# Performance work log

Measured on AMD Instinct MI355X. Metric: run time of the kernel, lower is better.

Reference implementation:

```python
import jax, jax.numpy as jnp
import numpy as np

B, T, C, H = 8, 1024, 768, 12
D = C // H  # head dim = 64


def setup_inputs() -> dict:
    key = jax.random.key(0)
    ks = jax.random.split(key, 5)
    x = jax.random.normal(ks[0], (B, T, C), dtype=jnp.float32)
    W_attn = jax.random.normal(ks[1], (C, 3 * C), dtype=jnp.float32) * 0.02
    b_attn = jnp.zeros((3 * C,), dtype=jnp.float32)
    W_proj = jax.random.normal(ks[2], (C, C), dtype=jnp.float32) * 0.02
    b_proj = jnp.zeros((C,), dtype=jnp.float32)
    return {"x": x, "W_attn": W_attn, "b_attn": b_attn, "W_proj": W_proj, "b_proj": b_proj}


def reference(x, W_attn, b_attn, W_proj, b_proj):
    Bx, Tx, Cx = x.shape
    qkv = x @ W_attn + b_attn                      # [B,T,3C]
    q, k, v = jnp.split(qkv, 3, axis=-1)           # each [B,T,C]
    # [B,T,C] -> [B,H,T,D]
    q = q.reshape(Bx, Tx, H, D).transpose(0, 2, 1, 3)
    k = k.reshape(Bx, Tx, H, D).transpose(0, 2, 1, 3)
    v = v.reshape(Bx, Tx, H, D).transpose(0, 2, 1, 3)
    scale = 1.0 / jnp.sqrt(jnp.asarray(D, dtype=x.dtype))
    att = jnp.einsum('bhqd,bhkd->bhqk', q, k) * scale   # [B,H,T,T]
    causal = jnp.tril(jnp.ones((Tx, Tx), dtype=bool))    # [T,T]
    att = jnp.where(causal[None, None, :, :], att, jnp.asarray(-jnp.inf, dtype=att.dtype))
    att = jax.nn.softmax(att, axis=-1)
    y = jnp.einsum('bhqk,bhkd->bhqd', att, v)            # [B,H,T,D]
    y = y.transpose(0, 2, 1, 3).reshape(Bx, Tx, Cx)      # [B,T,C]
    return y @ W_proj + b_proj
```

## Files before the change

kernel.cpp:

```cpp
#include <hip/hip_runtime.h>
#include <stdint.h>

typedef short short8 __attribute__((ext_vector_type(8)));
typedef float f32x4 __attribute__((ext_vector_type(4)));

__device__ __forceinline__ unsigned short f2bf(float f) {
    union { float f; uint32_t u; } v; v.f = f;
    uint32_t u = v.u;
    u += 0x7FFFu + ((u >> 16) & 1u);
    return (unsigned short)(u >> 16);
}

__device__ __forceinline__ void gload_lds16(const void* g, void* l) {
    __builtin_amdgcn_global_load_lds(
        (const __attribute__((address_space(1))) void*)g,
        (__attribute__((address_space(3))) void*)l, 16, 0, 0);
}

__global__ void k_f32_to_bf16(const float* __restrict__ in, unsigned short* __restrict__ out, int n4) {
    int i = blockIdx.x * blockDim.x + threadIdx.x;
    if (i < n4) {
        float4 f = ((const float4*)in)[i];
        ushort4 o;
        o.x = f2bf(f.x); o.y = f2bf(f.y); o.z = f2bf(f.z); o.w = f2bf(f.w);
        ((ushort4*)out)[i] = o;
    }
}

__global__ void k_transpose_f32_bf16(const float* __restrict__ in, unsigned short* __restrict__ out,
                                     int R, int Cc) {
    __shared__ float tile[32][33];
    int c0 = blockIdx.x * 32, r0 = blockIdx.y * 32;
    int tr = threadIdx.x / 32, c = threadIdx.x % 32;
#pragma unroll
    for (int rr = tr; rr < 32; rr += 8)
        tile[rr][c] = in[(size_t)(r0 + rr) * Cc + c0 + c];
    __syncthreads();
#pragma unroll
    for (int rr = tr; rr < 32; rr += 8)
        out[(size_t)(c0 + rr) * R + r0 + c] = f2bf(tile[c][rr]);
}

template<bool F32OUT, bool VSPLIT>
__global__ __launch_bounds__(256, 3)
void k_gemm_bt(const unsigned short* __restrict__ A, const unsigned short* __restrict__ BT,
               const float* __restrict__ bias, void* __restrict__ Cout,
               unsigned short* __restrict__ Vt,
               int M, int N, int K) {
    __shared__ unsigned short As[2][128][32];
    __shared__ unsigned short Bs[2][128][32];
    const int nbx = gridDim.x;
    const int total = nbx * gridDim.y;
    const int id = blockIdx.y * nbx + blockIdx.x;
    const int sw = (id & 7) * (total >> 3) + (id >> 3);
    const int m0 = (sw / nbx) * 128, n0 = (sw % nbx) * 128;
    const int t = threadIdx.x;
    const int w = t >> 6, l = t & 63;
    const int wm = (w >> 1) * 64, wn = (w & 1) * 64;
    const int lr = l & 15, lg = l >> 4;
    const int srow = w * 32 + (l >> 2);
    const int scol = (l & 3) * 8;
    const unsigned short* pa = &A [(size_t)(m0 + srow) * K + scol];
    const unsigned short* pb = &BT[(size_t)(n0 + srow) * K + scol];

    f32x4 acc[4][4];
#pragma unroll
    for (int i = 0; i < 4; ++i)
#pragma unroll
        for (int j = 0; j < 4; ++j)
#pragma unroll
            for (int r = 0; r < 4; ++r) acc[i][j][r] = 0.0f;

    for (int k0 = 0; k0 < K; k0 += 64) {
        __syncthreads();
        gload_lds16(pa + k0,                        &As[0][w * 32][0]);
        gload_lds16(pa + (size_t)16 * K + k0,       &As[0][w * 32 + 16][0]);
        gload_lds16(pa + k0 + 32,                   &As[1][w * 32][0]);
        gload_lds16(pa + (size_t)16 * K + k0 + 32,  &As[1][w * 32 + 16][0]);
        gload_lds16(pb + k0,                        &Bs[0][w * 32][0]);
        gload_lds16(pb + (size_t)16 * K + k0,       &Bs[0][w * 32 + 16][0]);
        gload_lds16(pb + k0 + 32,                   &Bs[1][w * 32][0]);
        gload_lds16(pb + (size_t)16 * K + k0 + 32,  &Bs[1][w * 32 + 16][0]);
        __syncthreads();
#pragma unroll
        for (int p = 0; p < 2; ++p) {
            short8 af[4], bfv[4];
#pragma unroll
            for (int f = 0; f < 4; ++f) {
                af [f] = *(const short8*)&As[p][wm + f * 16 + lr][lg * 8];
                bfv[f] = *(const short8*)&Bs[p][wn + f * 16 + lr][lg * 8];
            }
#pragma unroll
            for (int mf = 0; mf < 4; ++mf)
#pragma unroll
                for (int nf = 0; nf < 4; ++nf)
                    acc[mf][nf] = __builtin_amdgcn_mfma_f32_16x16x32_bf16(af[mf], bfv[nf], acc[mf][nf], 0, 0, 0);
        }
    }

#pragma unroll
    for (int mf = 0; mf < 4; ++mf)
#pragma unroll
        for (int nf = 0; nf < 4; ++nf) {
            int n = n0 + wn + nf * 16 + lr;
            int mbase = m0 + wm + mf * 16 + lg * 4;
            float bv = bias[n];
            if (VSPLIT && n >= 1536) {
                int hh = (n - 1536) >> 6, dd = (n - 1536) & 63;
                int bb = mbase >> 10, tt = mbase & 1023;
                ushort4 o;
                o.x = f2bf(acc[mf][nf][0] + bv);
                o.y = f2bf(acc[mf][nf][1] + bv);
                o.z = f2bf(acc[mf][nf][2] + bv);
                o.w = f2bf(acc[mf][nf][3] + bv);
                *(ushort4*)&Vt[(((size_t)bb * 12 + hh) * 64 + dd) * 1024 + tt] = o;
            } else {
#pragma unroll
                for (int r = 0; r < 4; ++r) {
                    float v = acc[mf][nf][r] + bv;
                    if (F32OUT) ((float*)Cout)[(size_t)(mbase + r) * N + n] = v;
                    else ((unsigned short*)Cout)[(size_t)(mbase + r) * N + n] = f2bf(v);
                }
            }
        }
}

__global__ __launch_bounds__(256, 3)
void k_attn(const unsigned short* __restrict__ qkv, const unsigned short* __restrict__ vt,
            unsigned short* __restrict__ y) {
    __shared__ unsigned short Ks[2][64][80];
    __shared__ unsigned short Vs[2][64][80];
    __shared__ unsigned short Ps[4][16][72];
    const int p = blockIdx.x;
    const int v = (p & 7) * 192 + (p >> 3);
    const int bh = v >> 4;
    const int qt = 15 - (v & 15);
    const int b = bh / 12, h = bh % 12;
    const int t = threadIdx.x, w = t >> 6, l = t & 63, lr = l & 15, lg = l >> 4;
    const int qw0 = qt * 64 + w * 16;

    const unsigned short* qbase = qkv + (size_t)b * 1024 * 2304 + h * 64;
    const unsigned short* kbase = qbase + 768;
    const unsigned short* vbase = vt + (size_t)bh * 64 * 1024;

    const int srow = t >> 2, scol = (t & 3) * 8;
    const unsigned short* kst = &kbase[(size_t)srow * 2304 + scol];
    const unsigned short* vst = &vbase[(size_t)srow * 1024 + scol];

    short8 qf0 = *(const short8*)&qbase[(size_t)(qw0 + lr) * 2304 + lg * 8];
    short8 qf1 = *(const short8*)&qbase[(size_t)(qw0 + lr) * 2304 + 32 + lg * 8];

    float l_lane[4];
    f32x4 o_acc[4];
#pragma unroll
    for (int r = 0; r < 4; ++r) l_lane[r] = 0.0f;
#pragma unroll
    for (int df = 0; df < 4; ++df)
#pragma unroll
        for (int r = 0; r < 4; ++r) o_acc[df][r] = 0.0f;

    {
        uint4 ka = *(const uint4*)(kst);
        uint4 kb = *(const uint4*)(kst + 32);
        uint4 va = *(const uint4*)(vst);
        uint4 vb = *(const uint4*)(vst + 32);
        *(uint4*)&Ks[0][srow][scol]      = ka;
        *(uint4*)&Ks[0][srow][scol + 32] = kb;
        *(uint4*)&Vs[0][srow][scol]      = va;
        *(uint4*)&Vs[0][srow][scol + 32] = vb;
    }
    __syncthreads();

    int cur = 0;
    for (int kti = 0; kti <= qt; ++kti) {
        const int kt = kti * 64;
        const bool diag = (kti == qt);
        const bool more = (kti < qt);
        uint4 nka, nkb, nva, nvb;
        if (more) {
            const int kn = kt + 64;
            nka = *(const uint4*)(kst + (size_t)kn * 2304);
            nkb = *(const uint4*)(kst + (size_t)kn * 2304 + 32);
            nva = *(const uint4*)(vst + kn);
            nvb = *(const uint4*)(vst + kn + 32);
        }

        f32x4 s[4];
        __builtin_amdgcn_s_setprio(1);
#pragma unroll
        for (int nf = 0; nf < 4; ++nf) {
            f32x4 z;
#pragma unroll
            for (int r = 0; r < 4; ++r) z[r] = 0.0f;
            if (!diag || nf <= w) {
                short8 kf0 = *(const short8*)&Ks[cur][nf * 16 + lr][lg * 8];
                short8 kf1 = *(const short8*)&Ks[cur][nf * 16 + lr][32 + lg * 8];
                z = __builtin_amdgcn_mfma_f32_16x16x32_bf16(qf0, kf0, z, 0, 0, 0);
                z = __builtin_amdgcn_mfma_f32_16x16x32_bf16(qf1, kf1, z, 0, 0, 0);
            }
            s[nf] = z;
        }
        __builtin_amdgcn_s_setprio(0);
        float pv[4][4];
#pragma unroll
        for (int nf = 0; nf < 4; ++nf) {
            int col = kt + nf * 16 + lr;
#pragma unroll
            for (int r = 0; r < 4; ++r) {
                bool ok = !diag || (nf < w) || (col <= qw0 + lg * 4 + r);
                float e = ok ? __expf(s[nf][r] * 0.125f - 8.0f) : 0.0f;
                pv[nf][r] = e;
                l_lane[r] += e;
            }
        }
#pragma unroll
        for (int nf = 0; nf < 4; ++nf)
#pragma unroll
            for (int r = 0; r < 4; ++r)
                Ps[w][lg * 4 + r][nf * 16 + lr] = f2bf(pv[nf][r]);
        short8 pf0 = *(const short8*)&Ps[w][lr][lg * 8];
        short8 pf1 = *(const short8*)&Ps[w][lr][32 + lg * 8];
        __builtin_amdgcn_s_setprio(1);
#pragma unroll
        for (int df = 0; df < 4; ++df) {
            short8 vf0 = *(const short8*)&Vs[cur][df * 16 + lr][lg * 8];
            short8 vf1 = *(const short8*)&Vs[cur][df * 16 + lr][32 + lg * 8];
            o_acc[df] = __builtin_amdgcn_mfma_f32_16x16x32_bf16(pf0, vf0, o_acc[df], 0, 0, 0);
            o_acc[df] = __builtin_amdgcn_mfma_f32_16x16x32_bf16(pf1, vf1, o_acc[df], 0, 0, 0);
        }
        __builtin_amdgcn_s_setprio(0);

        if (more) {
            *(uint4*)&Ks[cur ^ 1][srow][scol]      = nka;
            *(uint4*)&Ks[cur ^ 1][srow][scol + 32] = nkb;
            *(uint4*)&Vs[cur ^ 1][srow][scol]      = nva;
            *(uint4*)&Vs[cur ^ 1][srow][scol + 32] = nvb;
        }
        __syncthreads();
        cur ^= 1;
    }

#pragma unroll
    for (int r = 0; r < 4; ++r) {
        float s_ = l_lane[r];
#pragma unroll
        for (int d = 1; d < 16; d <<= 1) s_ += __shfl_xor(s_, d);
        float inv = 1.0f / s_;
        int row = qw0 + lg * 4 + r;
#pragma unroll
        for (int df = 0; df < 4; ++df)
            y[((size_t)b * 1024 + row) * 768 + h * 64 + df * 16 + lr] = f2bf(o_acc[df][r] * inv);
    }
}

extern "C" void kernel_launch(void* const* d_in, const int* in_sizes, int n_in,
                              void* d_out, int out_size, void* d_ws, size_t ws_size,
                              hipStream_t stream) {
    const float* x  = (const float*)d_in[0];
    const float* Wa = (const float*)d_in[1];
    const float* ba = (const float*)d_in[2];
    const float* Wp = (const float*)d_in[3];
    const float* bp = (const float*)d_in[4];
    float* out = (float*)d_out;

    char* ws = (char*)d_ws;
    unsigned short* qkv = (unsigned short*)ws;
    unsigned short* xb  = (unsigned short*)(ws + 37748736);
    unsigned short* WaT = (unsigned short*)(ws + 37748736 + 12582912);
    unsigned short* y   = xb;
    unsigned short* WpT = WaT;
    unsigned short* vtb = (unsigned short*)d_out;

    k_f32_to_bf16<<<6144, 256, 0, stream>>>(x, xb, 1572864);
    k_transpose_f32_bf16<<<dim3(72, 24), 256, 0, stream>>>(Wa, WaT, 768, 2304);
    k_gemm_bt<false, true><<<dim3(18, 64), 256, 0, stream>>>(xb, WaT, ba, qkv, vtb, 8192, 2304, 768);
    k_attn<<<1536, 256, 0, stream>>>(qkv, vtb, y);
    k_transpose_f32_bf16<<<dim3(24, 24), 256, 0, stream>>>(Wp, WpT, 768, 768);
    k_gemm_bt<true, false><<<dim3(6, 64), 256, 0, stream>>>(y, WpT, bp, out, nullptr, 8192, 768, 768);
}
```

Before: 119.4 us.

## Double-buffer GEMM LDS tiles and fuse input conversion/transposes into one kernel

```diff
diff --git a/kernel.cpp b/kernel.cpp
--- a/kernel.cpp
+++ b/kernel.cpp
@@ -17,20 +17,11 @@
         (__attribute__((address_space(3))) void*)l, 16, 0, 0);
 }
 
-__global__ void k_f32_to_bf16(const float* __restrict__ in, unsigned short* __restrict__ out, int n4) {
-    int i = blockIdx.x * blockDim.x + threadIdx.x;
-    if (i < n4) {
-        float4 f = ((const float4*)in)[i];
-        ushort4 o;
-        o.x = f2bf(f.x); o.y = f2bf(f.y); o.z = f2bf(f.z); o.w = f2bf(f.w);
-        ((ushort4*)out)[i] = o;
-    }
-}
-
-__global__ void k_transpose_f32_bf16(const float* __restrict__ in, unsigned short* __restrict__ out,
-                                     int R, int Cc) {
-    __shared__ float tile[32][33];
-    int c0 = blockIdx.x * 32, r0 = blockIdx.y * 32;
+__device__ __forceinline__ void transpose_body(const float* __restrict__ in,
+                                               unsigned short* __restrict__ out,
+                                               int R, int Cc, int bx, int by,
+                                               float (*tile)[33]) {
+    int c0 = bx * 32, r0 = by * 32;
     int tr = threadIdx.x / 32, c = threadIdx.x % 32;
 #pragma unroll
     for (int rr = tr; rr < 32; rr += 8)
@@ -41,14 +32,34 @@
         out[(size_t)(c0 + rr) * R + r0 + c] = f2bf(tile[c][rr]);
 }
 
+__global__ void k_prep(const float* __restrict__ x, unsigned short* __restrict__ xb,
+                       const float* __restrict__ Wa, unsigned short* __restrict__ WaT,
+                       const float* __restrict__ Wp, unsigned short* __restrict__ WpT) {
+    __shared__ float tile[32][33];
+    const int blk = blockIdx.x;
+    if (blk < 6144) {
+        int i = blk * 256 + threadIdx.x;
+        float4 f = ((const float4*)x)[i];
+        ushort4 o;
+        o.x = f2bf(f.x); o.y = f2bf(f.y); o.z = f2bf(f.z); o.w = f2bf(f.w);
+        ((ushort4*)xb)[i] = o;
+    } else if (blk < 6144 + 1728) {
+        int id = blk - 6144;
+        transpose_body(Wa, WaT, 768, 2304, id % 72, id / 72, tile);
+    } else {
+        int id = blk - 7872;
+        transpose_body(Wp, WpT, 768, 768, id % 24, id / 24, tile);
+    }
+}
+
 template<bool F32OUT, bool VSPLIT>
-__global__ __launch_bounds__(256, 3)
+__global__ __launch_bounds__(256, 2)
 void k_gemm_bt(const unsigned short* __restrict__ A, const unsigned short* __restrict__ BT,
                const float* __restrict__ bias, void* __restrict__ Cout,
                unsigned short* __restrict__ Vt,
                int M, int N, int K) {
-    __shared__ unsigned short As[2][128][32];
-    __shared__ unsigned short Bs[2][128][32];
+    __shared__ unsigned short As[2][2][128][32];
+    __shared__ unsigned short Bs[2][2][128][32];
     const int nbx = gridDim.x;
     const int total = nbx * gridDim.y;
     const int id = blockIdx.y * nbx + blockIdx.x;
@@ -71,24 +82,39 @@
 #pragma unroll
             for (int r = 0; r < 4; ++r) acc[i][j][r] = 0.0f;
 
+    {
+        gload_lds16(pa,                        &As[0][0][w * 32][0]);
+        gload_lds16(pa + (size_t)16 * K,       &As[0][0][w * 32 + 16][0]);
+        gload_lds16(pa + 32,                   &As[0][1][w * 32][0]);
+        gload_lds16(pa + (size_t)16 * K + 32,  &As[0][1][w * 32 + 16][0]);
+        gload_lds16(pb,                        &Bs[0][0][w * 32][0]);
+        gload_lds16(pb + (size_t)16 * K,       &Bs[0][0][w * 32 + 16][0]);
+        gload_lds16(pb + 32,                   &Bs[0][1][w * 32][0]);
+        gload_lds16(pb + (size_t)16 * K + 32,  &Bs[0][1][w * 32 + 16][0]);
+    }
+    __syncthreads();
+
+    int bufc = 0;
     for (int k0 = 0; k0 < K; k0 += 64) {
-        __syncthreads();
-        gload_lds16(pa + k0,                        &As[0][w * 32][0]);
-        gload_lds16(pa + (size_t)16 * K + k0,       &As[0][w * 32 + 16][0]);
-        gload_lds16(pa + k0 + 32,                   &As[1][w * 32][0]);
-        gload_lds16(pa + (size_t)16 * K + k0 + 32,  &As[1][w * 32 + 16][0]);
-        gload_lds16(pb + k0,                        &Bs[0][w * 32][0]);
-        gload_lds16(pb + (size_t)16 * K + k0,       &Bs[0][w * 32 + 16][0]);
-        gload_lds16(pb + k0 + 32,                   &Bs[1][w * 32][0]);
-        gload_lds16(pb + (size_t)16 * K + k0 + 32,  &Bs[1][w * 32 + 16][0]);
-        __syncthreads();
+        if (k0 + 64 < K) {
+            const int kn = k0 + 64;
+            const int bn = bufc ^ 1;
+            gload_lds16(pa + kn,                        &As[bn][0][w * 32][0]);
+            gload_lds16(pa + (size_t)16 * K + kn,       &As[bn][0][w * 32 + 16][0]);
+            gload_lds16(pa + kn + 32,                   &As[bn][1][w * 32][0]);
+            gload_lds16(pa + (size_t)16 * K + kn + 32,  &As[bn][1][w * 32 + 16][0]);
+            gload_lds16(pb + kn,                        &Bs[bn][0][w * 32][0]);
+            gload_lds16(pb + (size_t)16 * K + kn,       &Bs[bn][0][w * 32 + 16][0]);
+            gload_lds16(pb + kn + 32,                   &Bs[bn][1][w * 32][0]);
+            gload_lds16(pb + (size_t)16 * K + kn + 32,  &Bs[bn][1][w * 32 + 16][0]);
+        }
 #pragma unroll
         for (int p = 0; p < 2; ++p) {
             short8 af[4], bfv[4];
 #pragma unroll
             for (int f = 0; f < 4; ++f) {
-                af [f] = *(const short8*)&As[p][wm + f * 16 + lr][lg * 8];
-                bfv[f] = *(const short8*)&Bs[p][wn + f * 16 + lr][lg * 8];
+                af [f] = *(const short8*)&As[bufc][p][wm + f * 16 + lr][lg * 8];
+                bfv[f] = *(const short8*)&Bs[bufc][p][wn + f * 16 + lr][lg * 8];
             }
 #pragma unroll
             for (int mf = 0; mf < 4; ++mf)
@@ -96,6 +122,8 @@
                 for (int nf = 0; nf < 4; ++nf)
                     acc[mf][nf] = __builtin_amdgcn_mfma_f32_16x16x32_bf16(af[mf], bfv[nf], acc[mf][nf], 0, 0, 0);
         }
+        __syncthreads();
+        bufc ^= 1;
     }
 
 #pragma unroll
@@ -267,14 +295,12 @@
     unsigned short* qkv = (unsigned short*)ws;
     unsigned short* xb  = (unsigned short*)(ws + 37748736);
     unsigned short* WaT = (unsigned short*)(ws + 37748736 + 12582912);
+    unsigned short* WpT = (unsigned short*)(ws + 37748736 + 12582912 + 3538944);
     unsigned short* y   = xb;
-    unsigned short* WpT = WaT;
     unsigned short* vtb = (unsigned short*)d_out;
 
-    k_f32_to_bf16<<<6144, 256, 0, stream>>>(x, xb, 1572864);
-    k_transpose_f32_bf16<<<dim3(72, 24), 256, 0, stream>>>(Wa, WaT, 768, 2304);
+    k_prep<<<8448, 256, 0, stream>>>(x, xb, Wa, WaT, Wp, WpT);
     k_gemm_bt<false, true><<<dim3(18, 64), 256, 0, stream>>>(xb, WaT, ba, qkv, vtb, 8192, 2304, 768);
     k_attn<<<1536, 256, 0, stream>>>(qkv, vtb, y);
-    k_transpose_f32_bf16<<<dim3(24, 24), 256, 0, stream>>>(Wp, WpT, 768, 768);
     k_gemm_bt<true, false><<<dim3(6, 64), 256, 0, stream>>>(y, WpT, bp, out, nullptr, 8192, 768, 768);
 }
```

Result: slower. 126.2 us (+5.6%).

## Process two query tiles per attention block and merge prep kernels into one launch

Applied to the files above, without the earlier changes.

```diff
diff --git a/kernel.cpp b/kernel.cpp
--- a/kernel.cpp
+++ b/kernel.cpp
@@ -17,20 +17,11 @@
         (__attribute__((address_space(3))) void*)l, 16, 0, 0);
 }
 
-__global__ void k_f32_to_bf16(const float* __restrict__ in, unsigned short* __restrict__ out, int n4) {
-    int i = blockIdx.x * blockDim.x + threadIdx.x;
-    if (i < n4) {
-        float4 f = ((const float4*)in)[i];
-        ushort4 o;
-        o.x = f2bf(f.x); o.y = f2bf(f.y); o.z = f2bf(f.z); o.w = f2bf(f.w);
-        ((ushort4*)out)[i] = o;
-    }
-}
-
-__global__ void k_transpose_f32_bf16(const float* __restrict__ in, unsigned short* __restrict__ out,
-                                     int R, int Cc) {
-    __shared__ float tile[32][33];
-    int c0 = blockIdx.x * 32, r0 = blockIdx.y * 32;
+__device__ __forceinline__ void transpose_body(const float* __restrict__ in,
+                                               unsigned short* __restrict__ out,
+                                               int R, int Cc, int bx, int by,
+                                               float (*tile)[33]) {
+    int c0 = bx * 32, r0 = by * 32;
     int tr = threadIdx.x / 32, c = threadIdx.x % 32;
 #pragma unroll
     for (int rr = tr; rr < 32; rr += 8)
@@ -39,6 +30,26 @@
 #pragma unroll
     for (int rr = tr; rr < 32; rr += 8)
         out[(size_t)(c0 + rr) * R + r0 + c] = f2bf(tile[c][rr]);
+}
+
+__global__ void k_prep(const float* __restrict__ x, unsigned short* __restrict__ xb,
+                       const float* __restrict__ Wa, unsigned short* __restrict__ WaT,
+                       const float* __restrict__ Wp, unsigned short* __restrict__ WpT) {
+    __shared__ float tile[32][33];
+    const int blk = blockIdx.x;
+    if (blk < 6144) {
+        int i = blk * 256 + threadIdx.x;
+        float4 f = ((const float4*)x)[i];
+        ushort4 o;
+        o.x = f2bf(f.x); o.y = f2bf(f.y); o.z = f2bf(f.z); o.w = f2bf(f.w);
+        ((ushort4*)xb)[i] = o;
+    } else if (blk < 6144 + 1728) {
+        int id = blk - 6144;
+        transpose_body(Wa, WaT, 768, 2304, id % 72, id / 72, tile);
+    } else {
+        int id = blk - 7872;
+        transpose_body(Wp, WpT, 768, 768, id % 24, id / 24, tile);
+    }
 }
 
 template<bool F32OUT, bool VSPLIT>
@@ -132,12 +143,12 @@
     __shared__ unsigned short Vs[2][64][80];
     __shared__ unsigned short Ps[4][16][72];
     const int p = blockIdx.x;
-    const int v = (p & 7) * 192 + (p >> 3);
-    const int bh = v >> 4;
-    const int qt = 15 - (v & 15);
+    const int v = (p & 7) * 96 + (p >> 3);
+    const int bh = v >> 3;
+    const int qt = 7 - (v & 7);
     const int b = bh / 12, h = bh % 12;
     const int t = threadIdx.x, w = t >> 6, l = t & 63, lr = l & 15, lg = l >> 4;
-    const int qw0 = qt * 64 + w * 16;
+    const int q0 = qt * 128;
 
     const unsigned short* qbase = qkv + (size_t)b * 1024 * 2304 + h * 64;
     const unsigned short* kbase = qbase + 768;
@@ -147,17 +158,24 @@
     const unsigned short* kst = &kbase[(size_t)srow * 2304 + scol];
     const unsigned short* vst = &vbase[(size_t)srow * 1024 + scol];
 
-    short8 qf0 = *(const short8*)&qbase[(size_t)(qw0 + lr) * 2304 + lg * 8];
-    short8 qf1 = *(const short8*)&qbase[(size_t)(qw0 + lr) * 2304 + 32 + lg * 8];
-
-    float l_lane[4];
-    f32x4 o_acc[4];
-#pragma unroll
-    for (int r = 0; r < 4; ++r) l_lane[r] = 0.0f;
-#pragma unroll
-    for (int df = 0; df < 4; ++df)
-#pragma unroll
-        for (int r = 0; r < 4; ++r) o_acc[df][r] = 0.0f;
+    short8 qf[2][2];
+#pragma unroll
+    for (int g = 0; g < 2; ++g) {
+        const unsigned short* qrow = &qbase[(size_t)(q0 + g * 64 + w * 16 + lr) * 2304];
+        qf[g][0] = *(const short8*)&qrow[lg * 8];
+        qf[g][1] = *(const short8*)&qrow[32 + lg * 8];
+    }
+
+    float l_lane[2][4];
+    f32x4 o_acc[2][4];
+#pragma unroll
+    for (int g = 0; g < 2; ++g)
+#pragma unroll
+        for (int r = 0; r < 4; ++r) {
+            l_lane[g][r] = 0.0f;
+#pragma unroll
+            for (int df = 0; df < 4; ++df) o_acc[g][df][r] = 0.0f;
+        }
 
     {
         uint4 ka = *(const uint4*)(kst);
@@ -171,11 +189,11 @@
     }
     __syncthreads();
 
+    const int nkt = qt * 2 + 2;
     int cur = 0;
-    for (int kti = 0; kti <= qt; ++kti) {
+    for (int kti = 0; kti < nkt; ++kti) {
         const int kt = kti * 64;
-        const bool diag = (kti == qt);
-        const bool more = (kti < qt);
+        const bool more = (kti + 1 < nkt);
         uint4 nka, nkb, nva, nvb;
         if (more) {
             const int kn = kt + 64;
@@ -185,50 +203,57 @@
             nvb = *(const uint4*)(vst + kn + 32);
         }
 
-        f32x4 s[4];
-        __builtin_amdgcn_s_setprio(1);
-#pragma unroll
-        for (int nf = 0; nf < 4; ++nf) {
-            f32x4 z;
-#pragma unroll
-            for (int r = 0; r < 4; ++r) z[r] = 0.0f;
-            if (!diag || nf <= w) {
-                short8 kf0 = *(const short8*)&Ks[cur][nf * 16 + lr][lg * 8];
-                short8 kf1 = *(const short8*)&Ks[cur][nf * 16 + lr][32 + lg * 8];
-                z = __builtin_amdgcn_mfma_f32_16x16x32_bf16(qf0, kf0, z, 0, 0, 0);
-                z = __builtin_amdgcn_mfma_f32_16x16x32_bf16(qf1, kf1, z, 0, 0, 0);
-            }
-            s[nf] = z;
-        }
-        __builtin_amdgcn_s_setprio(0);
-        float pv[4][4];
-#pragma unroll
-        for (int nf = 0; nf < 4; ++nf) {
-            int col = kt + nf * 16 + lr;
-#pragma unroll
-            for (int r = 0; r < 4; ++r) {
-                bool ok = !diag || (nf < w) || (col <= qw0 + lg * 4 + r);
-                float e = ok ? __expf(s[nf][r] * 0.125f - 8.0f) : 0.0f;
-                pv[nf][r] = e;
-                l_lane[r] += e;
-            }
-        }
-#pragma unroll
-        for (int nf = 0; nf < 4; ++nf)
-#pragma unroll
-            for (int r = 0; r < 4; ++r)
-                Ps[w][lg * 4 + r][nf * 16 + lr] = f2bf(pv[nf][r]);
-        short8 pf0 = *(const short8*)&Ps[w][lr][lg * 8];
-        short8 pf1 = *(const short8*)&Ps[w][lr][32 + lg * 8];
-        __builtin_amdgcn_s_setprio(1);
-#pragma unroll
-        for (int df = 0; df < 4; ++df) {
-            short8 vf0 = *(const short8*)&Vs[cur][df * 16 + lr][lg * 8];
-            short8 vf1 = *(const short8*)&Vs[cur][df * 16 + lr][32 + lg * 8];
-            o_acc[df] = __builtin_amdgcn_mfma_f32_16x16x32_bf16(pf0, vf0, o_acc[df], 0, 0, 0);
-            o_acc[df] = __builtin_amdgcn_mfma_f32_16x16x32_bf16(pf1, vf1, o_acc[df], 0, 0, 0);
-        }
-        __builtin_amdgcn_s_setprio(0);
+#pragma unroll
+        for (int g = 0; g < 2; ++g) {
+            if (g == 0 && kti == nkt - 1) continue;
+            const bool diag = (kti == nkt - 2 + g);
+            const int qw0 = q0 + g * 64 + w * 16;
+
+            f32x4 s[4];
+            __builtin_amdgcn_s_setprio(1);
+#pragma unroll
+            for (int nf = 0; nf < 4; ++nf) {
+                f32x4 z;
+#pragma unroll
+                for (int r = 0; r < 4; ++r) z[r] = 0.0f;
+                if (!diag || nf <= w) {
+                    short8 kf0 = *(const short8*)&Ks[cur][nf * 16 + lr][lg * 8];
+                    short8 kf1 = *(const short8*)&Ks[cur][nf * 16 + lr][32 + lg * 8];
+                    z = __builtin_amdgcn_mfma_f32_16x16x32_bf16(qf[g][0], kf0, z, 0, 0, 0);
+                    z = __builtin_amdgcn_mfma_f32_16x16x32_bf16(qf[g][1], kf1, z, 0, 0, 0);
+                }
+                s[nf] = z;
+            }
+            __builtin_amdgcn_s_setprio(0);
+            float pv[4][4];
+#pragma unroll
+            for (int nf = 0; nf < 4; ++nf) {
+                int col = kt + nf * 16 + lr;
+#pragma unroll
+                for (int r = 0; r < 4; ++r) {
+                    bool ok = !diag || (nf < w) || (col <= qw0 + lg * 4 + r);
+                    float e = ok ? __expf(s[nf][r] * 0.125f - 8.0f) : 0.0f;
+                    pv[nf][r] = e;
+                    l_lane[g][r] += e;
+                }
+            }
+#pragma unroll
+            for (int nf = 0; nf < 4; ++nf)
+#pragma unroll
+                for (int r = 0; r < 4; ++r)
+                    Ps[w][lg * 4 + r][nf * 16 + lr] = f2bf(pv[nf][r]);
+            short8 pf0 = *(const short8*)&Ps[w][lr][lg * 8];
+            short8 pf1 = *(const short8*)&Ps[w][lr][32 + lg * 8];
+            __builtin_amdgcn_s_setprio(1);
+#pragma unroll
+            for (int df = 0; df < 4; ++df) {
+                short8 vf0 = *(const short8*)&Vs[cur][df * 16 + lr][lg * 8];
+                short8 vf1 = *(const short8*)&Vs[cur][df * 16 + lr][32 + lg * 8];
+                o_acc[g][df] = __builtin_amdgcn_mfma_f32_16x16x32_bf16(pf0, vf0, o_acc[g][df], 0, 0, 0);
+                o_acc[g][df] = __builtin_amdgcn_mfma_f32_16x16x32_bf16(pf1, vf1, o_acc[g][df], 0, 0, 0);
+            }
+            __builtin_amdgcn_s_setprio(0);
+        }
 
         if (more) {
             *(uint4*)&Ks[cur ^ 1][srow][scol]      = nka;
@@ -241,16 +266,18 @@
     }
 
 #pragma unroll
-    for (int r = 0; r < 4; ++r) {
-        float s_ = l_lane[r];
-#pragma unroll
-        for (int d = 1; d < 16; d <<= 1) s_ += __shfl_xor(s_, d);
-        float inv = 1.0f / s_;
-        int row = qw0 + lg * 4 + r;
-#pragma unroll
-        for (int df = 0; df < 4; ++df)
-            y[((size_t)b * 1024 + row) * 768 + h * 64 + df * 16 + lr] = f2bf(o_acc[df][r] * inv);
-    }
+    for (int g = 0; g < 2; ++g)
+#pragma unroll
+        for (int r = 0; r < 4; ++r) {
+            float s_ = l_lane[g][r];
+#pragma unroll
+            for (int d = 1; d < 16; d <<= 1) s_ += __shfl_xor(s_, d);
+            float inv = 1.0f / s_;
+            int row = q0 + g * 64 + w * 16 + lg * 4 + r;
+#pragma unroll
+            for (int df = 0; df < 4; ++df)
+                y[((size_t)b * 1024 + row) * 768 + h * 64 + df * 16 + lr] = f2bf(o_acc[g][df][r] * inv);
+        }
 }
 
 extern "C" void kernel_launch(void* const* d_in, const int* in_sizes, int n_in,
@@ -267,14 +294,12 @@
     unsigned short* qkv = (unsigned short*)ws;
     unsigned short* xb  = (unsigned short*)(ws + 37748736);
     unsigned short* WaT = (unsigned short*)(ws + 37748736 + 12582912);
+    unsigned short* WpT = (unsigned short*)(ws + 37748736 + 12582912 + 3538944);
     unsigned short* y   = xb;
-    unsigned short* WpT = WaT;
     unsigned short* vtb = (unsigned short*)d_out;
 
-    k_f32_to_bf16<<<6144, 256, 0, stream>>>(x, xb, 1572864);
-    k_transpose_f32_bf16<<<dim3(72, 24), 256, 0, stream>>>(Wa, WaT, 768, 2304);
+    k_prep<<<8448, 256, 0, stream>>>(x, xb, Wa, WaT, Wp, WpT);
     k_gemm_bt<false, true><<<dim3(18, 64), 256, 0, stream>>>(xb, WaT, ba, qkv, vtb, 8192, 2304, 768);
-    k_attn<<<1536, 256, 0, stream>>>(qkv, vtb, y);
-    k_transpose_f32_bf16<<<dim3(24, 24), 256, 0, stream>>>(Wp, WpT, 768, 768);
+    k_attn<<<768, 256, 0, stream>>>(qkv, vtb, y);
     k_gemm_bt<true, false><<<dim3(6, 64), 256, 0, stream>>>(y, WpT, bp, out, nullptr, 8192, 768, 768);
 }
```

New measurement: 119.2 us. Within noise of the previous version (-0.2%).
